# Optimization experiments

Hardware: AMD Instinct MI355X
Metric: run time of the kernel (lower is better)

The kernel has to match this reference:

```python
import jax, jax.numpy as jnp
from jax import lax
import numpy as np

DN = ('NCHW', 'OIHW', 'NCHW')
EPS = 1e-8
LRELU_SLOPE = 0.2
SQRT2 = np.float32(np.sqrt(2.0))


def _blur2d(x):
    # 5x5 binomial FIR, depthwise, padding=2, stride=1 (Blur2d(kernel_size=5, padding=2))
    k1 = jnp.array([1.0, 4.0, 6.0, 4.0, 1.0], dtype=x.dtype)
    k2 = jnp.outer(k1, k1)
    k2 = k2 / k2.sum()
    C = x.shape[1]
    kern = jnp.broadcast_to(k2, (C, 1, 5, 5))
    return lax.conv_general_dilated(x, kern, window_strides=(1, 1),
                                    padding=[(2, 2), (2, 2)],
                                    feature_group_count=C,
                                    dimension_numbers=DN)


def _second_moment_norm(x, g):
    # normalize by per-channel spatial second moment, learnable gain g [C]
    ms = jnp.mean(jnp.square(x), axis=(2, 3), keepdims=True)  # [B,C,1,1]
    return x * lax.rsqrt(ms + EPS) * g[None, :, None, None]


def _modulated_conv(x, w, b, style_w, style_b, s, stride, padding):
    # StyleGAN2 modulated conv with demodulation, grouped-conv batch trick
    B, I, H, W = x.shape
    O, _, kh, kw = w.shape
    scale = np.float32(1.0 / np.sqrt(I * kh * kw))
    style = s @ style_w.T + style_b[None, :]                      # [B, I]
    wm = scale * w[None] * style[:, None, :, None, None]          # [B,O,I,kh,kw]
    d = lax.rsqrt(jnp.sum(jnp.square(wm), axis=(2, 3, 4)) + EPS)  # [B,O]
    wm = wm * d[:, :, None, None, None]
    xg = x.reshape(1, B * I, H, W)
    wg = wm.reshape(B * O, I, kh, kw)
    out = lax.conv_general_dilated(xg, wg, window_strides=(stride, stride),
                                   padding=[(padding, padding), (padding, padding)],
                                   feature_group_count=B,
                                   dimension_numbers=DN)
    out = out.reshape(B, O, out.shape[2], out.shape[3])
    return out + b[None, :, None, None]


def setup_inputs() -> dict:
    key = jax.random.key(0)
    ks = jax.random.split(key, 5)
    B, I, O, S, H, W, K = 8, 256, 256, 512, 128, 128, 3
    x = jax.random.normal(ks[0], (B, I, H, W), dtype=jnp.float32)
    s = jax.random.normal(ks[1], (B, S), dtype=jnp.float32)
    conv_w = jax.random.normal(ks[2], (O, I, K, K), dtype=jnp.float32)
    conv_b = jnp.zeros((O,), dtype=jnp.float32)
    style_w = jax.random.normal(ks[3], (I, S), dtype=jnp.float32) / np.float32(np.sqrt(S))
    style_b = jnp.ones((I,), dtype=jnp.float32)  # StyleGAN2 init: bias=1
    norm_g = jnp.ones((I,), dtype=jnp.float32)
    return {"x": x, "s": s, "conv_w": conv_w, "conv_b": conv_b,
            "style_w": style_w, "style_b": style_b, "norm_g": norm_g}


def reference(x, s, conv_w, conv_b, style_w, style_b, norm_g):
    x = _blur2d(x)                                   # blur (stride != 1 path)
    x = _second_moment_norm(x, norm_g)               # second-moment norm
    x = _modulated_conv(x, conv_w, conv_b, style_w, style_b, s, stride=2, padding=1)
    x = jnp.where(x >= 0, x, LRELU_SLOPE * x) * SQRT2  # scaled LeakyReLU
    return x
```

## Files before the change

kernel.cpp:

```cpp
#include <hip/hip_runtime.h>
#include <hip/hip_bf16.h>
#include <math.h>

#define B 8
#define IC 256
#define OC 256
#define SDIM 512
#define H 128
#define W 128
#define OH 64
#define OW 64
#define EPS 1e-8f
#define SQRT2 1.41421356237309504880f
#define SCALE 0.02083333395421505f

#define RS 16640
#define PLANE 1081600

typedef unsigned short u16;
typedef unsigned int u32;
typedef __attribute__((ext_vector_type(8))) short s16x8;
typedef __attribute__((ext_vector_type(4))) float f32x4;

__global__ void style_kernel(const float* __restrict__ s,
                             const float* __restrict__ sw,
                             const float* __restrict__ sb,
                             float* __restrict__ style) {
    int i = blockIdx.x * 256 + threadIdx.x;
    int b = i >> 8, ic = i & 255;
    const float* sv = s + (size_t)b * SDIM;
    const float* wv = sw + (size_t)ic * SDIM;
    float sum = 0.f;
    for (int k = 0; k < SDIM; ++k) sum = fmaf(sv[k], wv[k], sum);
    style[i] = sum + sb[ic];
}

__global__ void wsq_kernel(const float* __restrict__ w, float* __restrict__ wsq) {
    int i = blockIdx.x * 256 + threadIdx.x;
    const float* p = w + (size_t)i * 9;
    float sum = 0.f;
    for (int k = 0; k < 9; ++k) sum = fmaf(p[k], p[k], sum);
    wsq[i] = sum;
}

__global__ void demod_kernel(const float* __restrict__ style,
                             const float* __restrict__ wsq,
                             float* __restrict__ demod,
                             float* __restrict__ ssq) {
    int i = blockIdx.x * 256 + threadIdx.x;
    int b = i >> 8, o = i & 255;
    const float* st = style + b * 256;
    const float* wq = wsq + (size_t)o * 256;
    float sum = 0.f;
    for (int ic = 0; ic < 256; ++ic) {
        float sv = st[ic];
        sum = fmaf(sv * sv, wq[ic], sum);
    }
    demod[i] = rsqrtf(SCALE * SCALE * sum + EPS);
    ssq[i] = 0.f;
}

__global__ __launch_bounds__(256) void blur_kernel(const float* __restrict__ x,
                                                   __hip_bfloat16* __restrict__ xblur,
                                                   float* __restrict__ ssq) {
    __shared__ float img[36][128];
    __shared__ float tmp[36][128];
    __shared__ float red[4];
    int t = threadIdx.x;
    int strip = blockIdx.x & 3;
    int bc = blockIdx.x >> 2;
    int r0 = strip * 32;
    const size_t base = (size_t)bc * (H * W);

    #pragma unroll
    for (int k = 0; k < 18; ++k) {
        int e = t + k * 256;
        int lr = e >> 7, c = e & 127;
        int gr = r0 - 2 + lr;
        img[lr][c] = (gr >= 0 && gr < H) ? x[base + (size_t)gr * W + c] : 0.f;
    }
    __syncthreads();
    #pragma unroll
    for (int k = 0; k < 18; ++k) {
        int e = t + k * 256;
        int lr = e >> 7, c = e & 127;
        float sum = 6.f * img[lr][c];
        sum += 4.f * ((c >= 1 ? img[lr][c - 1] : 0.f) + (c <= 126 ? img[lr][c + 1] : 0.f));
        sum += (c >= 2 ? img[lr][c - 2] : 0.f) + (c <= 125 ? img[lr][c + 2] : 0.f);
        tmp[lr][c] = sum;
    }
    __syncthreads();
    float ss = 0.f;
    #pragma unroll
    for (int k = 0; k < 16; ++k) {
        int e = t + k * 256;
        int lr = (e >> 7) + 2, c = e & 127;
        float sum = 6.f * tmp[lr][c] + 4.f * (tmp[lr - 1][c] + tmp[lr + 1][c])
                  + (tmp[lr - 2][c] + tmp[lr + 2][c]);
        sum *= (1.0f / 256.0f);
        ss = fmaf(sum, sum, ss);
        xblur[base + (size_t)(r0 + (e >> 7)) * W + c] = __float2bfloat16(sum);
    }
    for (int off = 32; off; off >>= 1) ss += __shfl_down(ss, off, 64);
    if ((t & 63) == 0) red[t >> 6] = ss;
    __syncthreads();
    if (t == 0) atomicAdd(&ssq[bc], red[0] + red[1] + red[2] + red[3]);
}

__global__ void factor_kernel(const float* __restrict__ ssq,
                              const float* __restrict__ style,
                              const float* __restrict__ g,
                              float* __restrict__ factor) {
    int i = blockIdx.x * 256 + threadIdx.x;
    int c = i & 255;
    float ms = ssq[i] * (1.0f / (H * W));
    factor[i] = rsqrtf(ms + EPS) * g[c] * style[i] * SCALE;
}

__global__ void wf_kernel(const float* __restrict__ w,
                          const float* __restrict__ demod,
                          const float* __restrict__ factor,
                          __hip_bfloat16* __restrict__ wf) {
    int bo = blockIdx.x;
    int b = bo >> 8, o = bo & 255;
    int ic = threadIdx.x;
    float m = demod[bo] * factor[(b << 8) + ic];
    const float* wp = w + ((size_t)o * 256 + ic) * 9;
    __hip_bfloat16* dst = wf + (size_t)bo * 2304 + ic;
    #pragma unroll
    for (int t = 0; t < 9; ++t)
        dst[t * 256] = __float2bfloat16(wp[t] * m);
}

__global__ void zeropad_kernel(__hip_bfloat16* __restrict__ xbp) {
    int p = blockIdx.x;
    int t = threadIdx.x;
    char* base = (char*)(xbp + (size_t)p * PLANE);
    uint4 z = {0u, 0u, 0u, 0u};
    for (int k = 0; k < 9; ++k) {
        int c = t + (k << 8);
        if (c < 2080) *(uint4*)(base + (size_t)c * 16) = z;
    }
    for (int k = 0; k < 8; ++k) {
        int c = t + (k << 8);
        int r = 1 + (c >> 5);
        int off = (c & 31) << 3;
        *(uint4*)(base + ((size_t)r * RS + off) * 2) = z;
    }
}

__global__ __launch_bounds__(256) void pack_kernel(const __hip_bfloat16* __restrict__ xblur,
                                                   __hip_bfloat16* __restrict__ xbp) {
    __shared__ u16 tile[64][66];
    int t = threadIdx.x;
    int w0 = blockIdx.x << 6;
    int ic0 = blockIdx.y << 6;
    int z = blockIdx.z;
    int b = z >> 7, h = z & 127;
    int ph = h & 1, r = h >> 1;

    #pragma unroll
    for (int k = 0; k < 2; ++k) {
        int c = t + (k << 8);
        int ic_l = c >> 3, wc = c & 7;
        uint4 v = *(const uint4*)(xblur + (((size_t)(b * 256 + ic0 + ic_l)) << 14)
                                  + (h << 7) + w0 + (wc << 3));
        u32* dst = (u32*)&tile[ic_l][wc << 3];
        const u32* sv = (const u32*)&v;
        dst[0] = sv[0]; dst[1] = sv[1]; dst[2] = sv[2]; dst[3] = sv[3];
    }
    __syncthreads();
    #pragma unroll
    for (int k = 0; k < 2; ++k) {
        int c = t + (k << 8);
        int w_l = c >> 3, icg = c & 7;
        int w = w0 + w_l;
        int pw = w & 1, col = w >> 1;
        u32 pk[4];
        #pragma unroll
        for (int q = 0; q < 4; ++q) {
            u32 lo = tile[(icg << 3) + 2 * q][w_l];
            u32 hi = tile[(icg << 3) + 2 * q + 1][w_l];
            pk[q] = lo | (hi << 16);
        }
        size_t off = (size_t)((b << 2) + (ph << 1) + pw) * PLANE
                   + (size_t)(r + 1) * RS + (size_t)(col + 1) * 256 + ic0 + (icg << 3);
        *(uint4*)(xbp + off) = *(const uint4*)pk;
    }
}

__device__ __forceinline__ void gl_lds16(const void* g, void* l) {
    __builtin_amdgcn_global_load_lds((const __attribute__((address_space(1))) u32*)g,
                                     (__attribute__((address_space(3))) u32*)l, 16, 0, 0);
}

__global__ __launch_bounds__(256, 2) void conv_kernel(const __hip_bfloat16* __restrict__ xbp,
                                                      const __hip_bfloat16* __restrict__ wf,
                                                      const float* __restrict__ bias,
                                                      float* __restrict__ out) {
    __shared__ char lds[16384];
    const int t = threadIdx.x;
    const int o0 = blockIdx.x << 7;
    const int n0 = blockIdx.y << 7;
    const int b  = blockIdx.z;
    const size_t bb = (size_t)b << 8;

    const int mA  = t >> 2;
    const int kgl = t & 3;
    const int kga = kgl ^ ((mA >> 1) & 3);
    size_t preA0 = (bb + o0 + mA) * 2304 + (kga << 3);
    size_t preA1 = preA0 + (size_t)64 * 2304;
    const int ow = mA & 63;
    size_t preB0 = (size_t)(blockIdx.y << 1) * RS + (size_t)ow * 256 + (kga << 3);
    size_t preB1 = preB0 + RS;
    char* dA0 = lds + t * 16;
    char* dA1 = lds + 4096 + t * 16;
    char* dB0 = lds + 8192 + t * 16;
    char* dB1 = lds + 12288 + t * 16;

    const int lane = t & 63, wave = t >> 6;
    const int lr = lane & 15, quad = lane >> 4;
    const int mb = (wave & 1) << 6;
    const int nb = (wave >> 1) << 6;
    const int fragoff = ((quad ^ ((lr >> 1) & 3)) << 4);

    f32x4 acc[4][4];
    #pragma unroll
    for (int i = 0; i < 4; ++i)
        #pragma unroll
        for (int j = 0; j < 4; ++j) acc[i][j] = (f32x4){0.f, 0.f, 0.f, 0.f};

    for (int kk = 0; kk < 72; ++kk) {
        int tap = kk >> 3;
        int ic0 = (kk & 7) << 5;
        int th = (tap * 11) >> 5;
        int tw = tap - th * 3;
        int ph  = (th == 1) ? 0 : 1;
        int dhp = (th == 0) ? 0 : 1;
        int pw  = (tw == 1) ? 0 : 1;
        int dwp = (tw == 0) ? 0 : 1;
        size_t boff = (size_t)((b << 2) + (ph << 1) + pw) * PLANE
                    + (size_t)dhp * RS + (dwp << 8) + ic0;
        size_t aoff = (size_t)kk << 5;

        __syncthreads();
        gl_lds16(wf + preA0 + aoff, dA0);
        gl_lds16(wf + preA1 + aoff, dA1);
        gl_lds16(xbp + preB0 + boff, dB0);
        gl_lds16(xbp + preB1 + boff, dB1);
        __syncthreads();

        s16x8 a[4], bf[4];
        #pragma unroll
        for (int i = 0; i < 4; ++i)
            a[i] = *(const s16x8*)(lds + ((mb + (i << 4) + lr) << 6) + fragoff);
        #pragma unroll
        for (int j = 0; j < 4; ++j)
            bf[j] = *(const s16x8*)(lds + 8192 + ((nb + (j << 4) + lr) << 6) + fragoff);
        #pragma unroll
        for (int i = 0; i < 4; ++i)
            #pragma unroll
            for (int j = 0; j < 4; ++j)
                acc[i][j] = __builtin_amdgcn_mfma_f32_16x16x32_bf16(a[i], bf[j], acc[i][j], 0, 0, 0);
    }

    float bi[4][4];
    #pragma unroll
    for (int i = 0; i < 4; ++i)
        #pragma unroll
        for (int rr = 0; rr < 4; ++rr)
            bi[i][rr] = bias[o0 + mb + (i << 4) + (quad << 2) + rr];
    #pragma unroll
    for (int i = 0; i < 4; ++i) {
        #pragma unroll
        for (int j = 0; j < 4; ++j) {
            #pragma unroll
            for (int rr = 0; rr < 4; ++rr) {
                int oc = o0 + mb + (i << 4) + (quad << 2) + rr;
                int n = n0 + nb + (j << 4) + lr;
                int oh = n >> 6, ow2 = n & 63;
                float v = acc[i][j][rr] + bi[i][rr];
                v = (v >= 0.f ? v : 0.2f * v) * SQRT2;
                out[((bb + oc) << 12) + (oh << 6) + ow2] = v;
            }
        }
    }
}

extern "C" void kernel_launch(void* const* d_in, const int* in_sizes, int n_in,
                              void* d_out, int out_size, void* d_ws, size_t ws_size,
                              hipStream_t stream) {
    const float* x   = (const float*)d_in[0];
    const float* s   = (const float*)d_in[1];
    const float* cw  = (const float*)d_in[2];
    const float* cb  = (const float*)d_in[3];
    const float* sw  = (const float*)d_in[4];
    const float* sb  = (const float*)d_in[5];
    const float* ng  = (const float*)d_in[6];
    float* out = (float*)d_out;

    char* ws = (char*)d_ws;
    __hip_bfloat16* xblur = (__hip_bfloat16*)ws;
    __hip_bfloat16* xbp   = (__hip_bfloat16*)(ws + 67108864);
    __hip_bfloat16* wfb   = (__hip_bfloat16*)(ws + 136331264);
    float* style  = (float*)(ws + 145768448);
    float* wsq    = style + 2048;
    float* demod  = wsq + 65536;
    float* ssq    = demod + 2048;
    float* factor = ssq + 2048;

    style_kernel<<<8, 256, 0, stream>>>(s, sw, sb, style);
    wsq_kernel<<<256, 256, 0, stream>>>(cw, wsq);
    demod_kernel<<<8, 256, 0, stream>>>(style, wsq, demod, ssq);
    blur_kernel<<<B * IC * 4, 256, 0, stream>>>(x, xblur, ssq);
    factor_kernel<<<8, 256, 0, stream>>>(ssq, style, ng, factor);
    wf_kernel<<<2048, 256, 0, stream>>>(cw, demod, factor, wfb);
    zeropad_kernel<<<32, 256, 0, stream>>>(xbp);
    pack_kernel<<<dim3(2, 4, 1024), 256, 0, stream>>>(xblur, xbp);
    conv_kernel<<<dim3(2, 32, 8), 256, 0, stream>>>(xbp, wfb, cb, out);
}
```

Baseline: 356.4 us.

## Fuse blur with bf16 packing into the conv layout and inline factor computation

The separate blur, factor and pack kernels are merged into one blurpack kernel that reads fp32 input, applies the separable 5x5 blur and writes directly into the phase-split, channel-interleaved padded bf16 layout that the conv kernel consumes. It also accumulates the per-channel sum of squares. The factor computation moves into wf_kernel. This removes the intermediate xblur buffer round trip through global memory and two kernel launches. The vertical pass result is now rounded to bf16 before the horizontal pass, which adds a small precision change.

```diff
diff --git a/kernel.cpp b/kernel.cpp
--- a/kernel.cpp
+++ b/kernel.cpp
@@ -60,71 +60,91 @@
     ssq[i] = 0.f;
 }
 
-__global__ __launch_bounds__(256) void blur_kernel(const float* __restrict__ x,
-                                                   __hip_bfloat16* __restrict__ xblur,
-                                                   float* __restrict__ ssq) {
-    __shared__ float img[36][128];
-    __shared__ float tmp[36][128];
-    __shared__ float red[4];
-    int t = threadIdx.x;
-    int strip = blockIdx.x & 3;
-    int bc = blockIdx.x >> 2;
-    int r0 = strip * 32;
-    const size_t base = (size_t)bc * (H * W);
-
-    #pragma unroll
-    for (int k = 0; k < 18; ++k) {
-        int e = t + k * 256;
-        int lr = e >> 7, c = e & 127;
-        int gr = r0 - 2 + lr;
-        img[lr][c] = (gr >= 0 && gr < H) ? x[base + (size_t)gr * W + c] : 0.f;
-    }
-    __syncthreads();
-    #pragma unroll
-    for (int k = 0; k < 18; ++k) {
-        int e = t + k * 256;
-        int lr = e >> 7, c = e & 127;
-        float sum = 6.f * img[lr][c];
-        sum += 4.f * ((c >= 1 ? img[lr][c - 1] : 0.f) + (c <= 126 ? img[lr][c + 1] : 0.f));
-        sum += (c >= 2 ? img[lr][c - 2] : 0.f) + (c <= 125 ? img[lr][c + 2] : 0.f);
-        tmp[lr][c] = sum;
-    }
-    __syncthreads();
-    float ss = 0.f;
-    #pragma unroll
-    for (int k = 0; k < 16; ++k) {
-        int e = t + k * 256;
-        int lr = (e >> 7) + 2, c = e & 127;
-        float sum = 6.f * tmp[lr][c] + 4.f * (tmp[lr - 1][c] + tmp[lr + 1][c])
-                  + (tmp[lr - 2][c] + tmp[lr + 2][c]);
-        sum *= (1.0f / 256.0f);
-        ss = fmaf(sum, sum, ss);
-        xblur[base + (size_t)(r0 + (e >> 7)) * W + c] = __float2bfloat16(sum);
-    }
-    for (int off = 32; off; off >>= 1) ss += __shfl_down(ss, off, 64);
-    if ((t & 63) == 0) red[t >> 6] = ss;
-    __syncthreads();
-    if (t == 0) atomicAdd(&ssq[bc], red[0] + red[1] + red[2] + red[3]);
-}
-
-__global__ void factor_kernel(const float* __restrict__ ssq,
-                              const float* __restrict__ style,
-                              const float* __restrict__ g,
-                              float* __restrict__ factor) {
-    int i = blockIdx.x * 256 + threadIdx.x;
-    int c = i & 255;
-    float ms = ssq[i] * (1.0f / (H * W));
-    factor[i] = rsqrtf(ms + EPS) * g[c] * style[i] * SCALE;
+__global__ __launch_bounds__(256, 3) void blurpack_kernel(const float* __restrict__ x,
+                                                          __hip_bfloat16* __restrict__ xbp,
+                                                          float* __restrict__ ssq) {
+    __shared__ float img[8][12][128];
+    __shared__ u16 vbuf[2][8][132];
+    const int t = threadIdx.x;
+    const int strip = blockIdx.x;
+    const int ic0 = blockIdx.y << 3;
+    const int b = blockIdx.z;
+
+    #pragma unroll
+    for (int k = 0; k < 12; ++k) {
+        int e = t + (k << 8);
+        int ch = e / 384;
+        int rem = e - ch * 384;
+        int r = rem >> 5, c4 = rem & 31;
+        int gr = (strip << 3) - 2 + r;
+        float4 v = {0.f, 0.f, 0.f, 0.f};
+        if (gr >= 0 && gr < H)
+            v = *(const float4*)(x + (((size_t)(b * 256 + ic0 + ch)) << 14) + (gr << 7) + (c4 << 2));
+        *(float4*)&img[ch][r][c4 << 2] = v;
+    }
+    if (t < 64) {
+        int hr = t >> 5, ch = (t >> 2) & 7, sl = t & 3;
+        vbuf[hr][ch][sl < 2 ? sl : 128 + sl] = 0;
+    }
+
+    const int hr = t >> 7;
+    const int c = t & 127;
+    const int wl = t & 63;
+    float ss[8] = {0.f, 0.f, 0.f, 0.f, 0.f, 0.f, 0.f, 0.f};
+
+    for (int pass = 0; pass < 4; ++pass) {
+        int h_l = (pass << 1) + hr;
+        __syncthreads();
+        #pragma unroll
+        for (int ch = 0; ch < 8; ++ch) {
+            float a0 = img[ch][h_l][c],     a1 = img[ch][h_l + 1][c],
+                  a2 = img[ch][h_l + 2][c], a3 = img[ch][h_l + 3][c],
+                  a4 = img[ch][h_l + 4][c];
+            float v = fmaf(6.f, a2, fmaf(4.f, a1 + a3, a0 + a4));
+            __hip_bfloat16 bb = __float2bfloat16(v);
+            vbuf[hr][ch][c + 2] = *(u16*)&bb;
+        }
+        __syncthreads();
+        uint4 q;
+        u16* qp = (u16*)&q;
+        #pragma unroll
+        for (int ch = 0; ch < 8; ++ch) {
+            float s0 = __uint_as_float(((u32)vbuf[hr][ch][c]) << 16);
+            float s1 = __uint_as_float(((u32)vbuf[hr][ch][c + 1]) << 16);
+            float s2 = __uint_as_float(((u32)vbuf[hr][ch][c + 2]) << 16);
+            float s3 = __uint_as_float(((u32)vbuf[hr][ch][c + 3]) << 16);
+            float s4 = __uint_as_float(((u32)vbuf[hr][ch][c + 4]) << 16);
+            float hs = fmaf(6.f, s2, fmaf(4.f, s1 + s3, s0 + s4)) * (1.0f / 256.0f);
+            ss[ch] = fmaf(hs, hs, ss[ch]);
+            __hip_bfloat16 ob = __float2bfloat16(hs);
+            qp[ch] = *(u16*)&ob;
+        }
+        size_t off = (size_t)((b << 2) + (hr << 1) + (c & 1)) * PLANE
+                   + (size_t)((strip << 2) + pass + 1) * RS
+                   + (size_t)((c >> 1) + 1) * 256 + ic0;
+        *(uint4*)(xbp + off) = q;
+    }
+
+    #pragma unroll
+    for (int ch = 0; ch < 8; ++ch) {
+        float v = ss[ch];
+        for (int o2 = 32; o2; o2 >>= 1) v += __shfl_down(v, o2, 64);
+        if (wl == 0) atomicAdd(&ssq[(b << 8) + ic0 + ch], v);
+    }
 }
 
 __global__ void wf_kernel(const float* __restrict__ w,
                           const float* __restrict__ demod,
-                          const float* __restrict__ factor,
+                          const float* __restrict__ ssq,
+                          const float* __restrict__ style,
+                          const float* __restrict__ g,
                           __hip_bfloat16* __restrict__ wf) {
     int bo = blockIdx.x;
     int b = bo >> 8, o = bo & 255;
     int ic = threadIdx.x;
-    float m = demod[bo] * factor[(b << 8) + ic];
+    float fac = rsqrtf(ssq[(b << 8) + ic] * (1.0f / 16384.0f) + EPS)
+              * g[ic] * style[(b << 8) + ic] * SCALE;
+    float m = demod[bo] * fac;
     const float* wp = w + ((size_t)o * 256 + ic) * 9;
     __hip_bfloat16* dst = wf + (size_t)bo * 2304 + ic;
     #pragma unroll
@@ -146,46 +166,6 @@
         int r = 1 + (c >> 5);
         int off = (c & 31) << 3;
         *(uint4*)(base + ((size_t)r * RS + off) * 2) = z;
-    }
-}
-
-__global__ __launch_bounds__(256) void pack_kernel(const __hip_bfloat16* __restrict__ xblur,
-                                                   __hip_bfloat16* __restrict__ xbp) {
-    __shared__ u16 tile[64][66];
-    int t = threadIdx.x;
-    int w0 = blockIdx.x << 6;
-    int ic0 = blockIdx.y << 6;
-    int z = blockIdx.z;
-    int b = z >> 7, h = z & 127;
-    int ph = h & 1, r = h >> 1;
-
-    #pragma unroll
-    for (int k = 0; k < 2; ++k) {
-        int c = t + (k << 8);
-        int ic_l = c >> 3, wc = c & 7;
-        uint4 v = *(const uint4*)(xblur + (((size_t)(b * 256 + ic0 + ic_l)) << 14)
-                                  + (h << 7) + w0 + (wc << 3));
-        u32* dst = (u32*)&tile[ic_l][wc << 3];
-        const u32* sv = (const u32*)&v;
-        dst[0] = sv[0]; dst[1] = sv[1]; dst[2] = sv[2]; dst[3] = sv[3];
-    }
-    __syncthreads();
-    #pragma unroll
-    for (int k = 0; k < 2; ++k) {
-        int c = t + (k << 8);
-        int w_l = c >> 3, icg = c & 7;
-        int w = w0 + w_l;
-        int pw = w & 1, col = w >> 1;
-        u32 pk[4];
-        #pragma unroll
-        for (int q = 0; q < 4; ++q) {
-            u32 lo = tile[(icg << 3) + 2 * q][w_l];
-            u32 hi = tile[(icg << 3) + 2 * q + 1][w_l];
-            pk[q] = lo | (hi << 16);
-        }
-        size_t off = (size_t)((b << 2) + (ph << 1) + pw) * PLANE
-                   + (size_t)(r + 1) * RS + (size_t)(col + 1) * 256 + ic0 + (icg << 3);
-        *(uint4*)(xbp + off) = *(const uint4*)pk;
     }
 }
 
@@ -300,22 +280,18 @@
     float* out = (float*)d_out;
 
     char* ws = (char*)d_ws;
-    __hip_bfloat16* xblur = (__hip_bfloat16*)ws;
-    __hip_bfloat16* xbp   = (__hip_bfloat16*)(ws + 67108864);
-    __hip_bfloat16* wfb   = (__hip_bfloat16*)(ws + 136331264);
-    float* style  = (float*)(ws + 145768448);
+    __hip_bfloat16* xbp = (__hip_bfloat16*)ws;
+    __hip_bfloat16* wfb = (__hip_bfloat16*)(ws + 69222400);
+    float* style  = (float*)(ws + 78659584);
     float* wsq    = style + 2048;
     float* demod  = wsq + 65536;
     float* ssq    = demod + 2048;
-    float* factor = ssq + 2048;
 
     style_kernel<<<8, 256, 0, stream>>>(s, sw, sb, style);
     wsq_kernel<<<256, 256, 0, stream>>>(cw, wsq);
     demod_kernel<<<8, 256, 0, stream>>>(style, wsq, demod, ssq);
-    blur_kernel<<<B * IC * 4, 256, 0, stream>>>(x, xblur, ssq);
-    factor_kernel<<<8, 256, 0, stream>>>(ssq, style, ng, factor);
-    wf_kernel<<<2048, 256, 0, stream>>>(cw, demod, factor, wfb);
+    blurpack_kernel<<<dim3(16, 32, 8), 256, 0, stream>>>(x, xbp, ssq);
+    wf_kernel<<<2048, 256, 0, stream>>>(cw, demod, ssq, style, ng, wfb);
     zeropad_kernel<<<32, 256, 0, stream>>>(xbp);
-    pack_kernel<<<dim3(2, 4, 1024), 256, 0, stream>>>(xblur, xbp);
     conv_kernel<<<dim3(2, 32, 8), 256, 0, stream>>>(xbp, wfb, cb, out);
 }
```

New measurement: 454.5 us. 1.28x slower.
